# Kernel optimization log

Measured on AMD Instinct MI355X. Metric: run time of the kernel, lower is better.

## Reference

```python
import jax, jax.numpy as jnp
import numpy as np

NUM_LAYERS = 8
HIDDEN = 1000
INPUT = 2


def _uniform(key, shape, bound):
    return jax.random.uniform(key, shape, jnp.float32, -bound, bound)


def setup_inputs() -> dict:
    key = jax.random.key(0)
    ks = jax.random.split(key, 12)
    bound = 1.0 / np.sqrt(HIDDEN)
    inp = {
        "input": jax.random.normal(ks[0], (INPUT,), jnp.float32),
        "hiddens": jax.random.normal(ks[1], (NUM_LAYERS, 1, HIDDEN), jnp.float32),
        # GRU params, PyTorch gate order (r, z, n)
        "W_ih0": _uniform(ks[2], (3 * HIDDEN, INPUT), bound),            # layer 0 input weights
        "W_ih": _uniform(ks[3], (NUM_LAYERS - 1, 3 * HIDDEN, HIDDEN), bound),  # layers 1..7
        "W_hh": _uniform(ks[4], (NUM_LAYERS, 3 * HIDDEN, HIDDEN), bound),
        "b_ih": _uniform(ks[5], (NUM_LAYERS, 3 * HIDDEN), bound),
        "b_hh": _uniform(ks[6], (NUM_LAYERS, 3 * HIDDEN), bound),
        # output head 1000 -> 1
        "W_out": _uniform(ks[7], (1, HIDDEN), bound),
        "b_out": _uniform(ks[8], (1,), bound),
    }
    return inp


def _gru_cell(x, h, Wih, Whh, bih, bhh):
    gi = Wih @ x + bih                      # (3H,)
    gh = Whh @ h + bhh                      # (3H,)
    ir, iz, i_n = jnp.split(gi, 3)
    hr, hz, h_n = jnp.split(gh, 3)
    r = jax.nn.sigmoid(ir + hr)
    z = jax.nn.sigmoid(iz + hz)
    n = jnp.tanh(i_n + r * h_n)
    return (1.0 - z) * n + z * h


def reference(input, hiddens, W_ih0, W_ih, W_hh, b_ih, b_hh, W_out, b_out):
    x = input.reshape(-1)                   # (2,) single timestep, batch=1
    h_prev = hiddens[:, 0, :]               # (L, H)
    new_h = []
    layer_in = x
    for l in range(NUM_LAYERS):
        Wih_l = W_ih0 if l == 0 else W_ih[l - 1]
        h_l = _gru_cell(layer_in, h_prev[l], Wih_l, W_hh[l], b_ih[l], b_hh[l])
        new_h.append(h_l)
        layer_in = h_l                      # no dropout (inference semantics)
    flow = (W_out @ layer_in + b_out).reshape(1, 1, 1)
    hiddens_prime = jnp.stack(new_h)[:, None, :]   # (L, 1, H)
    return flow, hiddens_prime
```

## Files before the change

### kernel.cpp

```cpp
#include <hip/hip_runtime.h>
#include <math.h>

#define HIDDEN 1000
#define K4 250

__device__ __forceinline__ float wave_dot1000(const float* __restrict__ w,
                                              const float* __restrict__ v,
                                              int lane) {
  const float4* w4 = reinterpret_cast<const float4*>(w);
  const float4* v4 = reinterpret_cast<const float4*>(v);
  float acc = 0.f;
  for (int c = lane; c < K4; c += 64) {
    float4 a = w4[c];
    float4 b = v4[c];
    acc = fmaf(a.x, b.x, acc);
    acc = fmaf(a.y, b.y, acc);
    acc = fmaf(a.z, b.z, acc);
    acc = fmaf(a.w, b.w, acc);
  }
  #pragma unroll
  for (int off = 32; off; off >>= 1) acc += __shfl_xor(acc, off);
  return acc;
}

__device__ __forceinline__ float sigmoidf_(float x) {
  return 1.f / (1.f + expf(-x));
}

__global__ void gru_phaseA(const float* __restrict__ x,
                           const float* __restrict__ hiddens,
                           const float* __restrict__ Wih0,
                           const float* __restrict__ Whh,
                           const float* __restrict__ bih,
                           const float* __restrict__ bhh,
                           float* __restrict__ gh_ws,
                           float* __restrict__ h_buf,
                           float* __restrict__ out)
{
  const int wave = threadIdx.x >> 6;
  const int lane = threadIdx.x & 63;
  const int b = blockIdx.x;

  if (b < 250) {
    const int j = b * 4 + wave;
    const float* h0 = hiddens;
    float ghr = wave_dot1000(Whh + (size_t)(j)         * HIDDEN, h0, lane) + bhh[j];
    float ghz = wave_dot1000(Whh + (size_t)(1000 + j)  * HIDDEN, h0, lane) + bhh[1000 + j];
    float ghn = wave_dot1000(Whh + (size_t)(2000 + j)  * HIDDEN, h0, lane) + bhh[2000 + j];
    if (lane == 0) {
      const float x0 = x[0], x1 = x[1];
      float gir = Wih0[2*j]          * x0 + Wih0[2*j+1]          * x1 + bih[j];
      float giz = Wih0[2*(1000+j)]   * x0 + Wih0[2*(1000+j)+1]   * x1 + bih[1000 + j];
      float gin = Wih0[2*(2000+j)]   * x0 + Wih0[2*(2000+j)+1]   * x1 + bih[2000 + j];
      float r = sigmoidf_(gir + ghr);
      float z = sigmoidf_(giz + ghz);
      float n = tanhf(gin + r * ghn);
      float h = (1.f - z) * n + z * h0[j];
      h_buf[j] = h;
      out[1 + j] = h;
    }
  } else {
    const int rg = (b - 250) * 4 + wave;
    const int l = rg / 3000 + 1;
    const int r = rg % 3000;
    const float* hl = hiddens + (size_t)l * HIDDEN;
    float gh = wave_dot1000(Whh + ((size_t)l * 3000 + r) * HIDDEN, hl, lane)
             + bhh[l * 3000 + r];
    if (lane == 0) gh_ws[rg] = gh;
  }
}

__global__ void gru_layer(const int l,
                          const float* __restrict__ hiddens,
                          const float* __restrict__ Wih,
                          const float* __restrict__ bih,
                          const float* __restrict__ gh_ws,
                          float* __restrict__ h_buf,
                          float* __restrict__ out)
{
  const int wave = threadIdx.x >> 6;
  const int lane = threadIdx.x & 63;
  const int j = blockIdx.x * 4 + wave;
  const float* hin = h_buf + (size_t)(l - 1) * HIDDEN;
  const float* W = Wih + (size_t)(l - 1) * 3000 * HIDDEN;

  float gir = wave_dot1000(W + (size_t)(j)        * HIDDEN, hin, lane) + bih[l*3000 + j];
  float giz = wave_dot1000(W + (size_t)(1000 + j) * HIDDEN, hin, lane) + bih[l*3000 + 1000 + j];
  float gin = wave_dot1000(W + (size_t)(2000 + j) * HIDDEN, hin, lane) + bih[l*3000 + 2000 + j];

  if (lane == 0) {
    float ghr = gh_ws[(l-1)*3000 + j];
    float ghz = gh_ws[(l-1)*3000 + 1000 + j];
    float ghn = gh_ws[(l-1)*3000 + 2000 + j];
    float hp  = hiddens[(size_t)l * HIDDEN + j];
    float r = sigmoidf_(gir + ghr);
    float z = sigmoidf_(giz + ghz);
    float n = tanhf(gin + r * ghn);
    float h = (1.f - z) * n + z * hp;
    h_buf[l * HIDDEN + j] = h;
    out[1 + l * HIDDEN + j] = h;
  }
}

__global__ void gru_flow(const float* __restrict__ Wout,
                         const float* __restrict__ bout,
                         const float* __restrict__ h_buf,
                         float* __restrict__ out)
{
  const int t = threadIdx.x;
  const float* h7 = h_buf + 7 * HIDDEN;
  float acc = 0.f;
  for (int i = t; i < HIDDEN; i += 256) acc += Wout[i] * h7[i];
  #pragma unroll
  for (int off = 32; off; off >>= 1) acc += __shfl_xor(acc, off);
  __shared__ float s[4];
  const int wave = t >> 6, lane = t & 63;
  if (lane == 0) s[wave] = acc;
  __syncthreads();
  if (t == 0) out[0] = s[0] + s[1] + s[2] + s[3] + bout[0];
}

extern "C" void kernel_launch(void* const* d_in, const int* in_sizes, int n_in,
                              void* d_out, int out_size, void* d_ws, size_t ws_size,
                              hipStream_t stream) {
  const float* x       = (const float*)d_in[0];
  const float* hiddens = (const float*)d_in[1];
  const float* Wih0    = (const float*)d_in[2];
  const float* Wih     = (const float*)d_in[3];
  const float* Whh     = (const float*)d_in[4];
  const float* bih     = (const float*)d_in[5];
  const float* bhh     = (const float*)d_in[6];
  const float* Wout    = (const float*)d_in[7];
  const float* bout    = (const float*)d_in[8];
  float* out   = (float*)d_out;
  float* gh_ws = (float*)d_ws;
  float* h_buf = gh_ws + 21000;

  gru_phaseA<<<5500, 256, 0, stream>>>(x, hiddens, Wih0, Whh, bih, bhh,
                                       gh_ws, h_buf, out);
  for (int l = 1; l < 8; ++l) {
    gru_layer<<<250, 256, 0, stream>>>(l, hiddens, Wih, bih, gh_ws, h_buf, out);
  }
  gru_flow<<<1, 256, 0, stream>>>(Wout, bout, h_buf, out);
}
```

Measured before the change: 71.92 us.

## Fuse all GRU layers into one cooperative kernel with grid syncs

Replaces the phase-A kernel, seven per-layer launches and the output-head kernel with a single cooperative kernel of 250 blocks of 768 threads. Each wave computes one gate row. The W_hh dot products for each layer are now done inside that layer's step alongside the W_ih dot, instead of all being precomputed up front. Layers are separated by grid.sync, which removes launch overhead and the gh workspace round trip. The cost is that the big W_hh traffic now sits on the serial critical path, interleaved with grid-wide barriers, rather than being spread across 5500 parallel blocks at the start.

```diff
diff --git a/kernel.cpp b/kernel.cpp
--- a/kernel.cpp
+++ b/kernel.cpp
@@ -1,123 +1,144 @@
 #include <hip/hip_runtime.h>
+#include <hip/hip_cooperative_groups.h>
 #include <math.h>
+
+namespace cg = cooperative_groups;
 
 #define HIDDEN 1000
 #define K4 250
-
-__device__ __forceinline__ float wave_dot1000(const float* __restrict__ w,
-                                              const float* __restrict__ v,
-                                              int lane) {
-  const float4* w4 = reinterpret_cast<const float4*>(w);
-  const float4* v4 = reinterpret_cast<const float4*>(v);
-  float acc = 0.f;
-  for (int c = lane; c < K4; c += 64) {
-    float4 a = w4[c];
-    float4 b = v4[c];
-    acc = fmaf(a.x, b.x, acc);
-    acc = fmaf(a.y, b.y, acc);
-    acc = fmaf(a.z, b.z, acc);
-    acc = fmaf(a.w, b.w, acc);
-  }
-  #pragma unroll
-  for (int off = 32; off; off >>= 1) acc += __shfl_xor(acc, off);
-  return acc;
-}
 
 __device__ __forceinline__ float sigmoidf_(float x) {
   return 1.f / (1.f + expf(-x));
 }
 
-__global__ void gru_phaseA(const float* __restrict__ x,
-                           const float* __restrict__ hiddens,
-                           const float* __restrict__ Wih0,
-                           const float* __restrict__ Whh,
-                           const float* __restrict__ bih,
-                           const float* __restrict__ bhh,
-                           float* __restrict__ gh_ws,
-                           float* __restrict__ h_buf,
-                           float* __restrict__ out)
-{
-  const int wave = threadIdx.x >> 6;
-  const int lane = threadIdx.x & 63;
-  const int b = blockIdx.x;
-
-  if (b < 250) {
-    const int j = b * 4 + wave;
-    const float* h0 = hiddens;
-    float ghr = wave_dot1000(Whh + (size_t)(j)         * HIDDEN, h0, lane) + bhh[j];
-    float ghz = wave_dot1000(Whh + (size_t)(1000 + j)  * HIDDEN, h0, lane) + bhh[1000 + j];
-    float ghn = wave_dot1000(Whh + (size_t)(2000 + j)  * HIDDEN, h0, lane) + bhh[2000 + j];
-    if (lane == 0) {
-      const float x0 = x[0], x1 = x[1];
-      float gir = Wih0[2*j]          * x0 + Wih0[2*j+1]          * x1 + bih[j];
-      float giz = Wih0[2*(1000+j)]   * x0 + Wih0[2*(1000+j)+1]   * x1 + bih[1000 + j];
-      float gin = Wih0[2*(2000+j)]   * x0 + Wih0[2*(2000+j)+1]   * x1 + bih[2000 + j];
-      float r = sigmoidf_(gir + ghr);
-      float z = sigmoidf_(giz + ghz);
-      float n = tanhf(gin + r * ghn);
-      float h = (1.f - z) * n + z * h0[j];
-      h_buf[j] = h;
-      out[1 + j] = h;
-    }
-  } else {
-    const int rg = (b - 250) * 4 + wave;
-    const int l = rg / 3000 + 1;
-    const int r = rg % 3000;
-    const float* hl = hiddens + (size_t)l * HIDDEN;
-    float gh = wave_dot1000(Whh + ((size_t)l * 3000 + r) * HIDDEN, hl, lane)
-             + bhh[l * 3000 + r];
-    if (lane == 0) gh_ws[rg] = gh;
+__device__ __forceinline__ float wave_dot1(const float4* __restrict__ w,
+                                           const float4* __restrict__ v,
+                                           int lane) {
+  float a = 0.f;
+  for (int c = lane; c < K4; c += 64) {
+    float4 x = w[c], y = v[c];
+    a = fmaf(x.x, y.x, a); a = fmaf(x.y, y.y, a);
+    a = fmaf(x.z, y.z, a); a = fmaf(x.w, y.w, a);
   }
+  #pragma unroll
+  for (int off = 32; off; off >>= 1) a += __shfl_xor(a, off);
+  return a;
 }
 
-__global__ void gru_layer(const int l,
-                          const float* __restrict__ hiddens,
-                          const float* __restrict__ Wih,
-                          const float* __restrict__ bih,
-                          const float* __restrict__ gh_ws,
-                          float* __restrict__ h_buf,
-                          float* __restrict__ out)
-{
-  const int wave = threadIdx.x >> 6;
-  const int lane = threadIdx.x & 63;
-  const int j = blockIdx.x * 4 + wave;
-  const float* hin = h_buf + (size_t)(l - 1) * HIDDEN;
-  const float* W = Wih + (size_t)(l - 1) * 3000 * HIDDEN;
-
-  float gir = wave_dot1000(W + (size_t)(j)        * HIDDEN, hin, lane) + bih[l*3000 + j];
-  float giz = wave_dot1000(W + (size_t)(1000 + j) * HIDDEN, hin, lane) + bih[l*3000 + 1000 + j];
-  float gin = wave_dot1000(W + (size_t)(2000 + j) * HIDDEN, hin, lane) + bih[l*3000 + 2000 + j];
-
-  if (lane == 0) {
-    float ghr = gh_ws[(l-1)*3000 + j];
-    float ghz = gh_ws[(l-1)*3000 + 1000 + j];
-    float ghn = gh_ws[(l-1)*3000 + 2000 + j];
-    float hp  = hiddens[(size_t)l * HIDDEN + j];
-    float r = sigmoidf_(gir + ghr);
-    float z = sigmoidf_(giz + ghz);
-    float n = tanhf(gin + r * ghn);
-    float h = (1.f - z) * n + z * hp;
-    h_buf[l * HIDDEN + j] = h;
-    out[1 + l * HIDDEN + j] = h;
+__device__ __forceinline__ void wave_dot2(const float4* __restrict__ w1,
+                                          const float4* __restrict__ v1,
+                                          const float4* __restrict__ w2,
+                                          const float4* __restrict__ v2,
+                                          int lane, float& d1, float& d2) {
+  float a1 = 0.f, a2 = 0.f;
+  for (int c = lane; c < K4; c += 64) {
+    float4 x1 = w1[c], y1 = v1[c];
+    float4 x2 = w2[c], y2 = v2[c];
+    a1 = fmaf(x1.x, y1.x, a1); a1 = fmaf(x1.y, y1.y, a1);
+    a1 = fmaf(x1.z, y1.z, a1); a1 = fmaf(x1.w, y1.w, a1);
+    a2 = fmaf(x2.x, y2.x, a2); a2 = fmaf(x2.y, y2.y, a2);
+    a2 = fmaf(x2.z, y2.z, a2); a2 = fmaf(x2.w, y2.w, a2);
   }
+  #pragma unroll
+  for (int off = 32; off; off >>= 1) {
+    a1 += __shfl_xor(a1, off);
+    a2 += __shfl_xor(a2, off);
+  }
+  d1 = a1; d2 = a2;
 }
 
-__global__ void gru_flow(const float* __restrict__ Wout,
-                         const float* __restrict__ bout,
-                         const float* __restrict__ h_buf,
-                         float* __restrict__ out)
+__global__ __launch_bounds__(768, 3)
+void gru_fused(const float* __restrict__ x,
+               const float* __restrict__ hiddens,
+               const float* __restrict__ Wih0,
+               const float* __restrict__ Wih,
+               const float* __restrict__ Whh,
+               const float* __restrict__ bih,
+               const float* __restrict__ bhh,
+               const float* __restrict__ Wout,
+               const float* __restrict__ bout,
+               float* __restrict__ h_buf,
+               float* __restrict__ out)
 {
-  const int t = threadIdx.x;
-  const float* h7 = h_buf + 7 * HIDDEN;
-  float acc = 0.f;
-  for (int i = t; i < HIDDEN; i += 256) acc += Wout[i] * h7[i];
-  #pragma unroll
-  for (int off = 32; off; off >>= 1) acc += __shfl_xor(acc, off);
-  __shared__ float s[4];
-  const int wave = t >> 6, lane = t & 63;
-  if (lane == 0) s[wave] = acc;
-  __syncthreads();
-  if (t == 0) out[0] = s[0] + s[1] + s[2] + s[3] + bout[0];
+  const int tid  = threadIdx.x;
+  const int wave = tid >> 6;
+  const int lane = tid & 63;
+  const int nidx = wave / 3;
+  const int g    = wave % 3;
+  const int j    = blockIdx.x * 4 + nidx;
+
+  __shared__ float s_gi[4][3];
+  __shared__ float s_gh[4][3];
+  __shared__ float sred[12];
+
+  cg::grid_group grid = cg::this_grid();
+
+  {
+    const float4* wrow = reinterpret_cast<const float4*>(
+        Whh + (size_t)(g * 1000 + j) * HIDDEN);
+    const float4* h0 = reinterpret_cast<const float4*>(hiddens);
+    float gh = wave_dot1(wrow, h0, lane);
+    if (lane == 0) s_gh[nidx][g] = gh + bhh[g * 1000 + j];
+    __syncthreads();
+    if (tid < 4) {
+      const int jj = blockIdx.x * 4 + tid;
+      const float x0 = x[0], x1v = x[1];
+      float gir = fmaf(Wih0[2*jj],          x0, Wih0[2*jj+1]          * x1v) + bih[jj];
+      float giz = fmaf(Wih0[2*(1000+jj)],   x0, Wih0[2*(1000+jj)+1]   * x1v) + bih[1000+jj];
+      float gin = fmaf(Wih0[2*(2000+jj)],   x0, Wih0[2*(2000+jj)+1]   * x1v) + bih[2000+jj];
+      float r = sigmoidf_(gir + s_gh[tid][0]);
+      float z = sigmoidf_(giz + s_gh[tid][1]);
+      float n = tanhf(gin + r * s_gh[tid][2]);
+      float h = (1.f - z) * n + z * hiddens[jj];
+      h_buf[jj] = h;
+      out[1 + jj] = h;
+    }
+  }
+
+  for (int l = 1; l < 8; ++l) {
+    grid.sync();
+    const float4* hin   = reinterpret_cast<const float4*>(h_buf   + (size_t)(l - 1) * HIDDEN);
+    const float4* hprev = reinterpret_cast<const float4*>(hiddens + (size_t)l * HIDDEN);
+    const float4* wgi = reinterpret_cast<const float4*>(
+        Wih + ((size_t)(l - 1) * 3000 + g * 1000 + j) * HIDDEN);
+    const float4* wgh = reinterpret_cast<const float4*>(
+        Whh + ((size_t)l * 3000 + g * 1000 + j) * HIDDEN);
+
+    float gi, gh;
+    wave_dot2(wgi, hin, wgh, hprev, lane, gi, gh);
+    if (lane == 0) {
+      s_gi[nidx][g] = gi + bih[l * 3000 + g * 1000 + j];
+      s_gh[nidx][g] = gh + bhh[l * 3000 + g * 1000 + j];
+    }
+    __syncthreads();
+    if (tid < 4) {
+      const int jj = blockIdx.x * 4 + tid;
+      float r = sigmoidf_(s_gi[tid][0] + s_gh[tid][0]);
+      float z = sigmoidf_(s_gi[tid][1] + s_gh[tid][1]);
+      float n = tanhf(s_gi[tid][2] + r * s_gh[tid][2]);
+      float h = (1.f - z) * n + z * hiddens[(size_t)l * HIDDEN + jj];
+      h_buf[l * HIDDEN + jj] = h;
+      out[1 + l * HIDDEN + jj] = h;
+    }
+    __syncthreads();
+  }
+
+  grid.sync();
+  if (blockIdx.x == 0) {
+    const float* h7 = h_buf + 7 * HIDDEN;
+    float acc = 0.f;
+    for (int i = tid; i < HIDDEN; i += 768) acc += Wout[i] * h7[i];
+    #pragma unroll
+    for (int off = 32; off; off >>= 1) acc += __shfl_xor(acc, off);
+    if (lane == 0) sred[wave] = acc;
+    __syncthreads();
+    if (tid == 0) {
+      float s = 0.f;
+      #pragma unroll
+      for (int i = 0; i < 12; ++i) s += sred[i];
+      out[0] = s + bout[0];
+    }
+  }
 }
 
 extern "C" void kernel_launch(void* const* d_in, const int* in_sizes, int n_in,
@@ -132,14 +153,12 @@
   const float* bhh     = (const float*)d_in[6];
   const float* Wout    = (const float*)d_in[7];
   const float* bout    = (const float*)d_in[8];
+  float* h_buf = (float*)d_ws;
   float* out   = (float*)d_out;
-  float* gh_ws = (float*)d_ws;
-  float* h_buf = gh_ws + 21000;
 
-  gru_phaseA<<<5500, 256, 0, stream>>>(x, hiddens, Wih0, Whh, bih, bhh,
-                                       gh_ws, h_buf, out);
-  for (int l = 1; l < 8; ++l) {
-    gru_layer<<<250, 256, 0, stream>>>(l, hiddens, Wih, bih, gh_ws, h_buf, out);
-  }
-  gru_flow<<<1, 256, 0, stream>>>(Wout, bout, h_buf, out);
+  void* args[] = {(void*)&x, (void*)&hiddens, (void*)&Wih0, (void*)&Wih,
+                  (void*)&Whh, (void*)&bih, (void*)&bhh, (void*)&Wout,
+                  (void*)&bout, (void*)&h_buf, (void*)&out};
+  hipLaunchCooperativeKernel((void*)gru_fused, dim3(250), dim3(768),
+                             args, 0, stream);
 }
```

Result: slower. 258.5 us (+259.4%).
